# Performance work log

Measured on AMD Instinct MI355X. Metric: run time of the kernel, lower is better.

The kernel has to match this reference:

```python
import jax, jax.numpy as jnp
import numpy as np

BST_DEPTH = 6
NB_SPLIT = 2**BST_DEPTH - 1          # 63 internal (split) nodes
NB_NODES = 2**(BST_DEPTH + 1) - 1    # 127 total nodes (heap layout)
SPLIT = np.arange(NB_SPLIT)
DESC_L = 2 * SPLIT + 1               # left children of split nodes
DESC_R = 2 * SPLIT + 2               # right children of split nodes


def setup_inputs() -> dict:
    key = jax.random.key(0)
    kx, ka = jax.random.split(key)
    x = jax.random.normal(kx, (131072, 512), dtype=jnp.float32)
    A = jax.random.uniform(ka, (NB_SPLIT, 512), dtype=jnp.float32)  # torch.rand init
    return {"x": x, "A": A}


def _compute_q(x, A):
    # XA[:, t] is the split score of internal node t; XA == XA[:, split_nodes]
    XA = x @ A.T                                         # [N, nb_split]
    q = jnp.ones((x.shape[0], NB_NODES), dtype=XA.dtype)  # [N, nb_nodes]
    # Seed children of each split node. NOTE: sequential semantics matter —
    # the right-child write reads q[:, SPLIT] AFTER the left-child write
    # (odd-indexed split nodes were just updated), matching torch in-place ops.
    q = q.at[:, DESC_L].set(jnp.minimum(q[:, SPLIT], XA))
    q = q.at[:, DESC_R].set(jnp.minimum(q[:, SPLIT], -XA))
    # Propagate the running min from parents down the tree, one sweep per level.
    for _ in range(BST_DEPTH):
        q = q.at[:, DESC_L].set(jnp.minimum(q[:, DESC_L], q[:, SPLIT]))
        q = q.at[:, DESC_R].set(jnp.minimum(q[:, DESC_R], q[:, SPLIT]))
    return q


def reference(x, A):
    q = _compute_q(x, A)
    z = jnp.clip(q, 0.0, 1.0)  # pruned=False: no QP pruning branch
    return z
```

## Files before the change

### kernel.cpp

```cpp
#include <hip/hip_runtime.h>
#include <hip/hip_bf16.h>
#include <cstdint>

#define KD 512
#define BM 128
#define NT 512
#define NSPLIT 63
#define NNODES 127
#define XB 6144
#define B_OFF 49152

typedef __attribute__((ext_vector_type(8))) short bf16x8;
typedef __attribute__((ext_vector_type(4))) float f32x4;

#define MFMA_B16(a, b, c) __builtin_amdgcn_mfma_f32_16x16x32_bf16(a, b, c, 0, 0, 0)
#define SCHED_FENCE() __builtin_amdgcn_sched_barrier(0)

static __device__ __forceinline__ unsigned short f2bf(float f) {
    return __builtin_bit_cast(unsigned short, __float2bfloat16(f));
}
static __device__ __forceinline__ float bf2f(unsigned short h) {
    return __builtin_bit_cast(float, (unsigned)h << 16);
}
static __device__ __forceinline__ unsigned pack2(float f0, float f1) {
    return (unsigned)f2bf(f0) | ((unsigned)f2bf(f1) << 16);
}

static __device__ __forceinline__ void cvt8(f32x4 a, f32x4 b, bf16x8& hi, bf16x8& lo) {
    const unsigned short h0 = f2bf(a[0]), h1 = f2bf(a[1]), h2 = f2bf(a[2]), h3 = f2bf(a[3]);
    const unsigned short h4 = f2bf(b[0]), h5 = f2bf(b[1]), h6 = f2bf(b[2]), h7 = f2bf(b[3]);
    uint4 H = make_uint4((unsigned)h0 | ((unsigned)h1 << 16), (unsigned)h2 | ((unsigned)h3 << 16),
                         (unsigned)h4 | ((unsigned)h5 << 16), (unsigned)h6 | ((unsigned)h7 << 16));
    uint4 L = make_uint4(pack2(a[0] - bf2f(h0), a[1] - bf2f(h1)),
                         pack2(a[2] - bf2f(h2), a[3] - bf2f(h3)),
                         pack2(b[0] - bf2f(h4), b[1] - bf2f(h5)),
                         pack2(b[2] - bf2f(h6), b[3] - bf2f(h7)));
    hi = __builtin_bit_cast(bf16x8, H);
    lo = __builtin_bit_cast(bf16x8, L);
}

static __device__ __forceinline__ void gload_lds16(const void* g, void* l) {
    __builtin_amdgcn_global_load_lds(
        (const __attribute__((address_space(1))) unsigned int*)g,
        (__attribute__((address_space(3))) unsigned int*)l, 16, 0, 0);
}

template<int N> static __device__ __forceinline__ void vmwait() {
    if constexpr (N == 6)      asm volatile("s_waitcnt vmcnt(6)" ::: "memory");
    else if constexpr (N == 4) asm volatile("s_waitcnt vmcnt(4)" ::: "memory");
    else if constexpr (N == 2) asm volatile("s_waitcnt vmcnt(2)" ::: "memory");
    else                       asm volatile("s_waitcnt vmcnt(0)" ::: "memory");
}

template<int T>
static __device__ __forceinline__ void tree_walk8(float qt, const float* __restrict__ srow,
                                                  float* __restrict__ zrow, int p8) {
    const float s  = srow[T];
    const float ql = fminf(qt, s);
    const float qr = fminf(qt, -s);
    if (((2 * T + 1) >> 4) == p8) zrow[2 * T + 1] = fminf(fmaxf(ql, 0.f), 1.f);
    if (((2 * T + 2) >> 4) == p8) zrow[2 * T + 2] = fminf(fmaxf(qr, 0.f), 1.f);
    if constexpr (2 * T + 1 < NSPLIT) tree_walk8<2 * T + 1>(ql, srow, zrow, p8);
    if constexpr (2 * T + 2 < NSPLIT) tree_walk8<2 * T + 2>(qr, srow, zrow, p8);
}

__global__ __launch_bounds__(256)
void lt_prep(const float* __restrict__ A, unsigned short* __restrict__ ws) {
    const int gid = blockIdx.x * 256 + threadIdx.x;
    const int row = gid >> 7;
    const int c4  = (gid & 127) << 2;
    f32x4 v = (f32x4)(0.f);
    if (row < NSPLIT)
        v = *reinterpret_cast<const f32x4*>(A + (size_t)row * KD + c4);
    const unsigned short h0 = f2bf(v[0]), h1 = f2bf(v[1]), h2 = f2bf(v[2]), h3 = f2bf(v[3]);
    uint2 hv = make_uint2((unsigned)h0 | ((unsigned)h1 << 16),
                          (unsigned)h2 | ((unsigned)h3 << 16));
    uint2 lv = make_uint2(pack2(v[0] - bf2f(h0), v[1] - bf2f(h1)),
                          pack2(v[2] - bf2f(h2), v[3] - bf2f(h3)));
    *reinterpret_cast<uint2*>(ws + row * KD + c4)         = hv;
    *reinterpret_cast<uint2*>(ws + 32768 + row * KD + c4) = lv;
}

template<int T>
static __device__ __forceinline__ void tiles(
        const float* xsrc, const unsigned short* bsrc,
        unsigned char* xw, unsigned char* bB, int bdoff,
        int va_off, int bo0, int bo1, f32x4 (&acc)[4]) {
    if constexpr ((T & 1) == 0) {
        SCHED_FENCE();
        vmwait<4>();
        SCHED_FENCE();
        __builtin_amdgcn_s_barrier();
        SCHED_FENCE();
        if constexpr (T / 2 + 1 < 8) {
            const unsigned short* bs = bsrc + (T / 2 + 1) * 64;
            unsigned char* bd = bB + ((T / 2 + 1) & 1) * 16384 + bdoff;
            gload_lds16(bs, bd);
            gload_lds16(bs + 8 * KD, bd + 1024);
        }
        SCHED_FENCE();
    }
    if constexpr (T + 2 < 16) {
        unsigned char* xd = xw + ((T + 2) % 3) * 2048;
        gload_lds16(xsrc + (T + 2) * 32, xd);
        gload_lds16(xsrc + (T + 2) * 32 + 8 * KD, xd + 1024);
    }
    SCHED_FENCE();
    vmwait<(T <= 13) ? 6 : ((T == 14) ? 2 : 0)>();
    SCHED_FENCE();

    const unsigned char* xbf = xw + (T % 3) * 2048;
    f32x4 va = *reinterpret_cast<const f32x4*>(xbf + va_off);
    f32x4 vb = *reinterpret_cast<const f32x4*>(xbf + (va_off ^ 16));
    bf16x8 ah, al;
    cvt8(va, vb, ah, al);

    const unsigned char* bb = bB + ((T >> 1) & 1) * 16384;
    const int bo = (T & 1) ? bo1 : bo0;
    bf16x8 b0 = *reinterpret_cast<const bf16x8*>(bb + bo);
    bf16x8 b1 = *reinterpret_cast<const bf16x8*>(bb + bo + 2048);
    bf16x8 b2 = *reinterpret_cast<const bf16x8*>(bb + bo + 4096);
    bf16x8 b3 = *reinterpret_cast<const bf16x8*>(bb + bo + 6144);
    acc[0] = MFMA_B16(ah, b0, acc[0]);
    acc[1] = MFMA_B16(ah, b1, acc[1]);
    acc[2] = MFMA_B16(ah, b2, acc[2]);
    acc[3] = MFMA_B16(ah, b3, acc[3]);
    acc[0] = MFMA_B16(al, b0, acc[0]);
    acc[1] = MFMA_B16(al, b1, acc[1]);
    acc[2] = MFMA_B16(al, b2, acc[2]);
    acc[3] = MFMA_B16(al, b3, acc[3]);
    b0 = *reinterpret_cast<const bf16x8*>(bb + 8192 + bo);
    b1 = *reinterpret_cast<const bf16x8*>(bb + 8192 + bo + 2048);
    b2 = *reinterpret_cast<const bf16x8*>(bb + 8192 + bo + 4096);
    b3 = *reinterpret_cast<const bf16x8*>(bb + 8192 + bo + 6144);
    acc[0] = MFMA_B16(ah, b0, acc[0]);
    acc[1] = MFMA_B16(ah, b1, acc[1]);
    acc[2] = MFMA_B16(ah, b2, acc[2]);
    acc[3] = MFMA_B16(ah, b3, acc[3]);

    if constexpr (T + 1 < 16)
        tiles<T + 1>(xsrc, bsrc, xw, bB, bdoff, va_off, bo0, bo1, acc);
}

__global__ __launch_bounds__(NT, 4)
void lt_mfma10(const float* __restrict__ x, const unsigned short* __restrict__ ws,
               float* __restrict__ out) {
    __shared__ __align__(16) unsigned char lds[81920];
    unsigned char* bB = lds + B_OFF;

    const int tid  = threadIdx.x;
    const int wave = tid >> 6;
    const int lane = tid & 63;
    const int fr   = lane & 15;
    const int g    = lane >> 4;
    const int r0   = blockIdx.x * BM;

    unsigned char* xw = lds + wave * XB;
    const float* xsrc = x + (size_t)(r0 + wave * 16 + (lane >> 3)) * KD
                          + (((lane & 7) ^ ((lane >> 3) & 7)) << 2);
    const int p  = wave >> 2;
    const int rq = wave & 3;
    const unsigned short* bsrc = ws + p * 32768
                                    + (size_t)(rq * 16 + (lane >> 3)) * KD
                                    + (((lane & 7) ^ ((lane >> 3) & 7)) << 3);
    const int bdoff = p * 8192 + rq * 2048;
    const int va_off = (fr << 7) + (((2 * g) ^ (fr & 7)) << 4);
    const int bo0    = (fr << 7) + ((g       ^ (fr & 7)) << 4);
    const int bo1    = (fr << 7) + (((4 + g) ^ (fr & 7)) << 4);

    f32x4 acc[4];
#pragma unroll
    for (int j = 0; j < 4; ++j) acc[j] = (f32x4)(0.f);

    gload_lds16(bsrc, bB + bdoff);
    gload_lds16(bsrc + 8 * KD, bB + bdoff + 1024);
    gload_lds16(xsrc, xw);
    gload_lds16(xsrc + 8 * KD, xw + 1024);
    gload_lds16(xsrc + 32, xw + 2048);
    gload_lds16(xsrc + 32 + 8 * KD, xw + 3072);
    SCHED_FENCE();

    tiles<0>(xsrc, bsrc, xw, bB, bdoff, va_off, bo0, bo1, acc);

    float* warea = reinterpret_cast<float*>(xw);
    float* zw    = warea + 520;
    const int o  = lane >> 3;
    const int p8 = lane & 7;

#pragma unroll
    for (int s = 0; s < 2; ++s) {
        if ((g >> 1) == s) {
#pragma unroll
            for (int nf = 0; nf < 4; ++nf)
#pragma unroll
                for (int rg = 0; rg < 4; ++rg)
                    warea[((g & 1) * 4 + rg) * 65 + nf * 16 + fr] = acc[nf][rg];
        }
        const float* srow = warea + o * 65;
        float* zrow = zw + o * NNODES;
        if (p8 == 0) zrow[0] = 1.f;
        tree_walk8<0>(1.f, srow, zrow, p8);

        float* og = out + (size_t)(r0 + wave * 16 + s * 8) * NNODES;
#pragma unroll
        for (int j = 0; j < 4; ++j) {
            const int idx = j * 64 + lane;
            if (idx < 254)
                *reinterpret_cast<f32x4*>(og + idx * 4) =
                    *reinterpret_cast<const f32x4*>(zw + idx * 4);
        }
    }
}

extern "C" void kernel_launch(void* const* d_in, const int* in_sizes, int n_in,
                              void* d_out, int out_size, void* d_ws, size_t ws_size,
                              hipStream_t stream) {
    const float* x = (const float*)d_in[0];
    const float* A = (const float*)d_in[1];
    float* out = (float*)d_out;
    unsigned short* ws = (unsigned short*)d_ws;
    const int nrows = in_sizes[0] / KD;
    lt_prep<<<dim3(32), dim3(256), 0, stream>>>(A, ws);
    lt_mfma10<<<dim3(nrows / BM), dim3(NT), 0, stream>>>(x, ws, out);
}
```

Measured before the change: 82.21 us.

## Keep full bf16 A split in LDS and stream x directly into registers

The GEMM kernel now loads the entire pre-split hi/lo bf16 copy of A (128 KB, with an XOR swizzle applied in the prep kernel) into LDS once per block. It reads x straight from global memory into registers with a four-deep register prefetch instead of staging it through LDS. Block size doubles to 1024 threads covering 256 rows, and the per-tile barriers and vmcnt waits are gone. The aim is to remove LDS staging traffic and synchronisation for x. In exchange, the large LDS footprint limits occupancy to one block per CU, and the direct global x loads are less coalesced.

```diff
diff --git a/kernel.cpp b/kernel.cpp
--- a/kernel.cpp
+++ b/kernel.cpp
@@ -3,12 +3,10 @@
 #include <cstdint>
 
 #define KD 512
-#define BM 128
-#define NT 512
+#define BM 256
+#define NT 1024
 #define NSPLIT 63
 #define NNODES 127
-#define XB 6144
-#define B_OFF 49152
 
 typedef __attribute__((ext_vector_type(8))) short bf16x8;
 typedef __attribute__((ext_vector_type(4))) float f32x4;
@@ -45,13 +43,6 @@
         (__attribute__((address_space(3))) unsigned int*)l, 16, 0, 0);
 }
 
-template<int N> static __device__ __forceinline__ void vmwait() {
-    if constexpr (N == 6)      asm volatile("s_waitcnt vmcnt(6)" ::: "memory");
-    else if constexpr (N == 4) asm volatile("s_waitcnt vmcnt(4)" ::: "memory");
-    else if constexpr (N == 2) asm volatile("s_waitcnt vmcnt(2)" ::: "memory");
-    else                       asm volatile("s_waitcnt vmcnt(0)" ::: "memory");
-}
-
 template<int T>
 static __device__ __forceinline__ void tree_walk8(float qt, const float* __restrict__ srow,
                                                   float* __restrict__ zrow, int p8) {
@@ -67,60 +58,46 @@
 __global__ __launch_bounds__(256)
 void lt_prep(const float* __restrict__ A, unsigned short* __restrict__ ws) {
     const int gid = blockIdx.x * 256 + threadIdx.x;
-    const int row = gid >> 7;
-    const int c4  = (gid & 127) << 2;
-    f32x4 v = (f32x4)(0.f);
-    if (row < NSPLIT)
-        v = *reinterpret_cast<const f32x4*>(A + (size_t)row * KD + c4);
-    const unsigned short h0 = f2bf(v[0]), h1 = f2bf(v[1]), h2 = f2bf(v[2]), h3 = f2bf(v[3]);
-    uint2 hv = make_uint2((unsigned)h0 | ((unsigned)h1 << 16),
-                          (unsigned)h2 | ((unsigned)h3 << 16));
-    uint2 lv = make_uint2(pack2(v[0] - bf2f(h0), v[1] - bf2f(h1)),
-                          pack2(v[2] - bf2f(h2), v[3] - bf2f(h3)));
-    *reinterpret_cast<uint2*>(ws + row * KD + c4)         = hv;
-    *reinterpret_cast<uint2*>(ws + 32768 + row * KD + c4) = lv;
+    const int r   = gid >> 6;
+    const int sk  = gid & 63;
+    const int k   = sk << 3;
+    f32x4 a = (f32x4)(0.f), b = (f32x4)(0.f);
+    if (r < NSPLIT) {
+        a = *reinterpret_cast<const f32x4*>(A + (size_t)r * KD + k);
+        b = *reinterpret_cast<const f32x4*>(A + (size_t)r * KD + k + 4);
+    }
+    bf16x8 hi, lo;
+    cvt8(a, b, hi, lo);
+    const int sl = sk ^ (r & 7);
+    unsigned short* p = ws + r * 512 + sl * 8;
+    *reinterpret_cast<bf16x8*>(p)         = hi;
+    *reinterpret_cast<bf16x8*>(p + 32768) = lo;
 }
 
 template<int T>
 static __device__ __forceinline__ void tiles(
-        const float* xsrc, const unsigned short* bsrc,
-        unsigned char* xw, unsigned char* bB, int bdoff,
-        int va_off, int bo0, int bo1, f32x4 (&acc)[4]) {
-    if constexpr ((T & 1) == 0) {
-        SCHED_FENCE();
-        vmwait<4>();
-        SCHED_FENCE();
-        __builtin_amdgcn_s_barrier();
-        SCHED_FENCE();
-        if constexpr (T / 2 + 1 < 8) {
-            const unsigned short* bs = bsrc + (T / 2 + 1) * 64;
-            unsigned char* bd = bB + ((T / 2 + 1) & 1) * 16384 + bdoff;
-            gload_lds16(bs, bd);
-            gload_lds16(bs + 8 * KD, bd + 1024);
-        }
-        SCHED_FENCE();
-    }
-    if constexpr (T + 2 < 16) {
-        unsigned char* xd = xw + ((T + 2) % 3) * 2048;
-        gload_lds16(xsrc + (T + 2) * 32, xd);
-        gload_lds16(xsrc + (T + 2) * 32 + 8 * KD, xd + 1024);
-    }
+        const float* xsl, const unsigned char* lds, int fr, int g,
+        f32x4& v0a, f32x4& v0b, f32x4& v1a, f32x4& v1b,
+        f32x4& v2a, f32x4& v2b, f32x4& v3a, f32x4& v3b, f32x4 (&acc)[4]) {
+    constexpr int C = T & 3;
+    f32x4 ca = (C == 0) ? v0a : (C == 1) ? v1a : (C == 2) ? v2a : v3a;
+    f32x4 cb = (C == 0) ? v0b : (C == 1) ? v1b : (C == 2) ? v2b : v3b;
+    bf16x8 ah, al;
+    cvt8(ca, cb, ah, al);
     SCHED_FENCE();
-    vmwait<(T <= 13) ? 6 : ((T == 14) ? 2 : 0)>();
+    if constexpr (T + 4 < 16) {
+        f32x4& na = (C == 0) ? v0a : (C == 1) ? v1a : (C == 2) ? v2a : v3a;
+        f32x4& nb = (C == 0) ? v0b : (C == 1) ? v1b : (C == 2) ? v2b : v3b;
+        na = *reinterpret_cast<const f32x4*>(xsl + (T + 4) * 32);
+        nb = *reinterpret_cast<const f32x4*>(xsl + (T + 4) * 32 + 4);
+    }
     SCHED_FENCE();
 
-    const unsigned char* xbf = xw + (T % 3) * 2048;
-    f32x4 va = *reinterpret_cast<const f32x4*>(xbf + va_off);
-    f32x4 vb = *reinterpret_cast<const f32x4*>(xbf + (va_off ^ 16));
-    bf16x8 ah, al;
-    cvt8(va, vb, ah, al);
-
-    const unsigned char* bb = bB + ((T >> 1) & 1) * 16384;
-    const int bo = (T & 1) ? bo1 : bo0;
-    bf16x8 b0 = *reinterpret_cast<const bf16x8*>(bb + bo);
-    bf16x8 b1 = *reinterpret_cast<const bf16x8*>(bb + bo + 2048);
-    bf16x8 b2 = *reinterpret_cast<const bf16x8*>(bb + bo + 4096);
-    bf16x8 b3 = *reinterpret_cast<const bf16x8*>(bb + bo + 6144);
+    const int so = fr * 1024 + (((T << 2) + g) ^ (fr & 7)) * 16;
+    bf16x8 b0 = *reinterpret_cast<const bf16x8*>(lds + so);
+    bf16x8 b1 = *reinterpret_cast<const bf16x8*>(lds + 16384 + so);
+    bf16x8 b2 = *reinterpret_cast<const bf16x8*>(lds + 32768 + so);
+    bf16x8 b3 = *reinterpret_cast<const bf16x8*>(lds + 49152 + so);
     acc[0] = MFMA_B16(ah, b0, acc[0]);
     acc[1] = MFMA_B16(ah, b1, acc[1]);
     acc[2] = MFMA_B16(ah, b2, acc[2]);
@@ -129,24 +106,24 @@
     acc[1] = MFMA_B16(al, b1, acc[1]);
     acc[2] = MFMA_B16(al, b2, acc[2]);
     acc[3] = MFMA_B16(al, b3, acc[3]);
-    b0 = *reinterpret_cast<const bf16x8*>(bb + 8192 + bo);
-    b1 = *reinterpret_cast<const bf16x8*>(bb + 8192 + bo + 2048);
-    b2 = *reinterpret_cast<const bf16x8*>(bb + 8192 + bo + 4096);
-    b3 = *reinterpret_cast<const bf16x8*>(bb + 8192 + bo + 6144);
+    b0 = *reinterpret_cast<const bf16x8*>(lds + 65536 + so);
+    b1 = *reinterpret_cast<const bf16x8*>(lds + 65536 + 16384 + so);
+    b2 = *reinterpret_cast<const bf16x8*>(lds + 65536 + 32768 + so);
+    b3 = *reinterpret_cast<const bf16x8*>(lds + 65536 + 49152 + so);
     acc[0] = MFMA_B16(ah, b0, acc[0]);
     acc[1] = MFMA_B16(ah, b1, acc[1]);
     acc[2] = MFMA_B16(ah, b2, acc[2]);
     acc[3] = MFMA_B16(ah, b3, acc[3]);
 
     if constexpr (T + 1 < 16)
-        tiles<T + 1>(xsrc, bsrc, xw, bB, bdoff, va_off, bo0, bo1, acc);
+        tiles<T + 1>(xsl, lds, fr, g,
+                     v0a, v0b, v1a, v1b, v2a, v2b, v3a, v3b, acc);
 }
 
 __global__ __launch_bounds__(NT, 4)
-void lt_mfma10(const float* __restrict__ x, const unsigned short* __restrict__ ws,
+void lt_mfma13(const float* __restrict__ x, const unsigned short* __restrict__ ws,
                float* __restrict__ out) {
-    __shared__ __align__(16) unsigned char lds[81920];
-    unsigned char* bB = lds + B_OFF;
+    __shared__ __align__(16) unsigned char lds[131072];
 
     const int tid  = threadIdx.x;
     const int wave = tid >> 6;
@@ -155,34 +132,37 @@
     const int g    = lane >> 4;
     const int r0   = blockIdx.x * BM;
 
-    unsigned char* xw = lds + wave * XB;
-    const float* xsrc = x + (size_t)(r0 + wave * 16 + (lane >> 3)) * KD
-                          + (((lane & 7) ^ ((lane >> 3) & 7)) << 2);
-    const int p  = wave >> 2;
-    const int rq = wave & 3;
-    const unsigned short* bsrc = ws + p * 32768
-                                    + (size_t)(rq * 16 + (lane >> 3)) * KD
-                                    + (((lane & 7) ^ ((lane >> 3) & 7)) << 3);
-    const int bdoff = p * 8192 + rq * 2048;
-    const int va_off = (fr << 7) + (((2 * g) ^ (fr & 7)) << 4);
-    const int bo0    = (fr << 7) + ((g       ^ (fr & 7)) << 4);
-    const int bo1    = (fr << 7) + (((4 + g) ^ (fr & 7)) << 4);
+    const float* xsl = x + (size_t)(r0 + wave * 16 + fr) * KD + g * 8;
+
+    {
+        const unsigned char* bsrc = (const unsigned char*)ws + wave * 8192 + lane * 16;
+        unsigned char* bdst = lds + wave * 8192;
+#pragma unroll
+        for (int i = 0; i < 8; ++i)
+            gload_lds16(bsrc + i * 1024, bdst + i * 1024);
+    }
+    SCHED_FENCE();
 
     f32x4 acc[4];
 #pragma unroll
     for (int j = 0; j < 4; ++j) acc[j] = (f32x4)(0.f);
 
-    gload_lds16(bsrc, bB + bdoff);
-    gload_lds16(bsrc + 8 * KD, bB + bdoff + 1024);
-    gload_lds16(xsrc, xw);
-    gload_lds16(xsrc + 8 * KD, xw + 1024);
-    gload_lds16(xsrc + 32, xw + 2048);
-    gload_lds16(xsrc + 32 + 8 * KD, xw + 3072);
-    SCHED_FENCE();
-
-    tiles<0>(xsrc, bsrc, xw, bB, bdoff, va_off, bo0, bo1, acc);
-
-    float* warea = reinterpret_cast<float*>(xw);
+    f32x4 v0a = *reinterpret_cast<const f32x4*>(xsl);
+    f32x4 v0b = *reinterpret_cast<const f32x4*>(xsl + 4);
+    f32x4 v1a = *reinterpret_cast<const f32x4*>(xsl + 32);
+    f32x4 v1b = *reinterpret_cast<const f32x4*>(xsl + 36);
+    f32x4 v2a = *reinterpret_cast<const f32x4*>(xsl + 64);
+    f32x4 v2b = *reinterpret_cast<const f32x4*>(xsl + 68);
+    f32x4 v3a = *reinterpret_cast<const f32x4*>(xsl + 96);
+    f32x4 v3b = *reinterpret_cast<const f32x4*>(xsl + 100);
+
+    __syncthreads();
+
+    tiles<0>(xsl, lds, fr, g, v0a, v0b, v1a, v1b, v2a, v2b, v3a, v3b, acc);
+
+    __syncthreads();
+
+    float* warea = reinterpret_cast<float*>(lds + wave * 8192);
     float* zw    = warea + 520;
     const int o  = lane >> 3;
     const int p8 = lane & 7;
@@ -220,6 +200,6 @@
     float* out = (float*)d_out;
     unsigned short* ws = (unsigned short*)d_ws;
     const int nrows = in_sizes[0] / KD;
-    lt_prep<<<dim3(32), dim3(256), 0, stream>>>(A, ws);
-    lt_mfma10<<<dim3(nrows / BM), dim3(NT), 0, stream>>>(x, ws, out);
-}
+    lt_prep<<<dim3(16), dim3(256), 0, stream>>>(A, ws);
+    lt_mfma13<<<dim3(nrows / BM), dim3(NT), 0, stream>>>(x, ws, out);
+}
```

Result: slower. 94.29 us (+14.7%).
